# Optimization experiments

Measured on AMD Instinct MI355X. Metric: run time of the kernel, lower is better.

## Reference

```python
import jax, jax.numpy as jnp
import numpy as np

L, HID, NH, DH, OUT = 20, 512, 8, 64, 1000
NPAT, PS = 14, 16
IN_DIM = 3 * PS * PS          # 768
SEQ = NPAT * NPAT + 1         # 197
BATCH = 64
EPS = 1e-5


def _pos_embeddings(seq_len, d):
    # sin(i/10000^(j/d)) for even j, cos(i/10000^((j-1)/d)) for odd j
    i = jnp.arange(seq_len, dtype=jnp.float32)[:, None]
    j = jnp.arange(d)
    je = (j - (j % 2)).astype(jnp.float32)
    ang = i / jnp.power(10000.0, je / d)
    return jnp.where(j % 2 == 0, jnp.sin(ang), jnp.cos(ang))


def _layernorm(x, g, b):
    m = jnp.mean(x, axis=-1, keepdims=True)
    v = jnp.mean(jnp.square(x - m), axis=-1, keepdims=True)
    return (x - m) * jax.lax.rsqrt(v + EPS) * g + b


def setup_inputs() -> dict:
    key = jax.random.key(0)
    ks = jax.random.split(key, 12)
    r = lambda k, sh: jax.random.normal(k, sh, dtype=jnp.float32) * 0.02
    return {
        "x": jax.random.normal(ks[0], (BATCH, 3, 224, 224), dtype=jnp.float32),
        "embed_W": r(ks[1], (IN_DIM, HID)),
        "embed_b": jnp.zeros((HID,), jnp.float32),
        "cls": r(ks[2], (HID,)),
        "ln1_g": jnp.ones((L, HID), jnp.float32),
        "ln1_b": jnp.zeros((L, HID), jnp.float32),
        "qW": r(ks[3], (L, NH, DH, DH)),
        "qb": jnp.zeros((L, NH, DH), jnp.float32),
        "kW": r(ks[4], (L, NH, DH, DH)),
        "kb": jnp.zeros((L, NH, DH), jnp.float32),
        "vW": r(ks[5], (L, NH, DH, DH)),
        "vb": jnp.zeros((L, NH, DH), jnp.float32),
        "ln2_g": jnp.ones((L, HID), jnp.float32),
        "ln2_b": jnp.zeros((L, HID), jnp.float32),
        "mlp1_W": r(ks[6], (L, HID, 4 * HID)),
        "mlp1_b": jnp.zeros((L, 4 * HID), jnp.float32),
        "mlp2_W": r(ks[7], (L, 4 * HID, HID)),
        "mlp2_b": jnp.zeros((L, HID), jnp.float32),
        "head_W": r(ks[8], (HID, OUT)),
        "head_b": jnp.zeros((OUT,), jnp.float32),
    }


def reference(x, embed_W, embed_b, cls, ln1_g, ln1_b, qW, qb, kW, kb, vW, vb,
              ln2_g, ln2_b, mlp1_W, mlp1_b, mlp2_W, mlp2_b, head_W, head_b):
    n = x.shape[0]
    # patchify: [n,3,224,224] -> [n,196,768], flatten order (c, ph, pw)
    p = x.reshape(n, 3, NPAT, PS, NPAT, PS)
    p = p.transpose(0, 2, 4, 1, 3, 5).reshape(n, NPAT * NPAT, IN_DIM)
    tokens = p @ embed_W + embed_b                      # [n,196,HID]
    cls_tok = jnp.broadcast_to(cls, (n, 1, HID))
    h = jnp.concatenate([cls_tok, tokens], axis=1)      # [n,197,HID]
    h = h + _pos_embeddings(SEQ, HID)

    scale = 1.0 / jnp.sqrt(jnp.float32(DH))

    def step(h, params):
        (g1, b1, qw, qb_, kw, kb_, vw, vb_, g2, b2, w1, b1m, w2, b2m) = params
        y = _layernorm(h, g1, b1)                       # [n,S,HID]
        yh = y.reshape(n, SEQ, NH, DH)
        # torch Linear: out = seq @ W.T + b; qw stored as [NH, out, in]
        q = jnp.einsum('nshd,hed->nshe', yh, qw) + qb_
        k = jnp.einsum('nshd,hed->nshe', yh, kw) + kb_
        v = jnp.einsum('nshd,hed->nshe', yh, vw) + vb_
        att = jax.nn.softmax(jnp.einsum('nqhd,nkhd->nhqk', q, k) * scale, axis=-1)
        o = jnp.einsum('nhqk,nkhd->nqhd', att, v).reshape(n, SEQ, HID)
        h = h + o
        z = _layernorm(h, g2, b2)
        z = jax.nn.gelu(z @ w1 + b1m, approximate=False) @ w2 + b2m
        return h + z, None

    params = (ln1_g, ln1_b, qW, qb, kW, kb, vW, vb,
              ln2_g, ln2_b, mlp1_W, mlp1_b, mlp2_W, mlp2_b)
    h, _ = jax.lax.scan(step, h, params)
    logits = h[:, 0] @ head_W + head_b
    return jax.nn.softmax(logits, axis=-1)
```

## Files before the change

### kernel.cpp

```cpp
#include <hip/hip_runtime.h>
#include <hip/hip_bf16.h>
#include <math.h>

#define LAY 20
#define HID 512
#define NH 8
#define DH 64
#define OUTC 1000
#define SEQ 197
#define SPAD 224
#define BATCH 64
#define TT (BATCH*SEQ)
#define M2 12800
#define NPTOK (BATCH*196)
#define IN_DIM 768

typedef __attribute__((ext_vector_type(8))) short bf16x8;
typedef __attribute__((ext_vector_type(4))) float f32x4;

__device__ __forceinline__ ushort f2bf(float f){
  __hip_bfloat16 h = __float2bfloat16(f);
  return *(ushort*)&h;
}
__device__ __forceinline__ float bf2f(ushort u){
  __hip_bfloat16 h = *(__hip_bfloat16*)&u;
  return __bfloat162float(h);
}

__device__ __forceinline__ float posemb(int i, int j){
  float je = (float)(j & ~1);
  float ang = (float)i * powf(10000.0f, -je * (1.0f/(float)HID));
  return (j & 1) ? cosf(ang) : sinf(ang);
}

__device__ __forceinline__ float gelu_exact(float x){
  return 0.5f * x * (1.0f + erff(x * 0.70710678118654752f));
}

__device__ __forceinline__ void gld_lds16(const ushort* g, ushort* l){
  __builtin_amdgcn_global_load_lds((const __attribute__((address_space(1))) void*)g,
                                   (__attribute__((address_space(3))) void*)l, 16, 0, 0);
}

__global__ __launch_bounds__(512)
void pos_kernel(float* __restrict__ pos){
  int i = blockIdx.x, j = threadIdx.x;
  pos[(size_t)i*HID + j] = posemb(i, j);
}

__global__ __launch_bounds__(256)
void convt_kernel(const float* __restrict__ src, ushort* __restrict__ dst,
                  int R, int C){
  __shared__ float tile[32][33];
  const float* s = src + (size_t)blockIdx.z * R * C;
  ushort* d      = dst + (size_t)blockIdx.z * R * C;
  int r0 = blockIdx.y * 32, c0 = blockIdx.x * 32;
  int tc = threadIdx.x & 31, tr = threadIdx.x >> 5;
  #pragma unroll
  for (int i = 0; i < 4; ++i)
    tile[tr + i*8][tc] = s[(size_t)(r0 + tr + i*8)*C + c0 + tc];
  __syncthreads();
  #pragma unroll
  for (int i = 0; i < 4; ++i)
    d[(size_t)(c0 + tr + i*8)*R + r0 + tc] = f2bf(tile[tc][tr + i*8]);
}

__global__ __launch_bounds__(256)
void cvt_kernel(const float* __restrict__ src, ushort* __restrict__ dst, int count){
  int idx = blockIdx.x * 256 + threadIdx.x;
  if (idx < count) dst[idx] = f2bf(src[idx]);
}

__global__ __launch_bounds__(256)
void patchify_kernel(const float* __restrict__ x, ushort* __restrict__ p){
  int idx = blockIdx.x * 256 + threadIdx.x;
  int r   = idx / 768, cdx = idx - r * 768;
  int n   = r / 196,  pp  = r - n * 196;
  int pr  = pp / 14,  pc  = pp - pr * 14;
  int c   = cdx >> 8, rem = cdx & 255;
  int ph  = rem >> 4, pw  = rem & 15;
  p[idx] = f2bf(x[ (((size_t)(n*3 + c)*224) + pr*16 + ph)*224 + pc*16 + pw ]);
}

__global__ __launch_bounds__(512)
void cls_kernel(const float* __restrict__ cls, const float* __restrict__ pos,
                float* __restrict__ h){
  int n = blockIdx.x, e = threadIdx.x;
  h[(size_t)n*SEQ*HID + e] = cls[e] + pos[e];
}

template<int EPI>
__global__ __launch_bounds__(256, 4)
void gemm_pipe(const ushort* __restrict__ A, const ushort* __restrict__ Bt,
               const float* __restrict__ bias, void* __restrict__ Cv,
               int K, int N, int Mreal, int NBX, const float* __restrict__ pos){
  constexpr int BM = 128, BN = 128;
  constexpr int MF = 4, NF = 4;
  constexpr int TBS = 16384;
  constexpr int ES = 76;
  __shared__ char lds[2*TBS];

  int t = threadIdx.x, lane = t & 63, wave = t >> 6;
  int wr = wave >> 1, wn = wave & 1;
  int l16 = lane & 15, g = lane >> 4;

  int NB = gridDim.x;
  int q8 = NB >> 3, r8 = NB & 7;
  int xcd = blockIdx.x & 7, i8 = blockIdx.x >> 3;
  int swz = (xcd < r8 ? xcd*(q8+1) : r8*(q8+1) + (xcd-r8)*q8) + i8;
  int rb = (swz / NBX) * BM, cb = (swz % NBX) * BN;

  const int srow = t >> 2;
  const int kel  = ((t & 3) ^ ((srow >> 1) & 3)) * 8;
  const ushort* pA[2]; const ushort* pB[2];
  #pragma unroll
  for (int q = 0; q < 2; ++q){
    pA[q] = A  + (size_t)(rb + q*64 + srow)*K + kel;
    pB[q] = Bt + (size_t)(cb + q*64 + srow)*K + kel;
  }
  const int sdst = t*16;

  const int sx = (l16 >> 1) & 3;
  int aoff[MF], boff[NF];
  #pragma unroll
  for (int mf = 0; mf < MF; ++mf)
    aoff[mf] = (wr*64 + mf*16 + l16)*64 + ((g ^ sx) << 4);
  #pragma unroll
  for (int nf = 0; nf < NF; ++nf)
    boff[nf] = 8192 + (wn*64 + nf*16 + l16)*64 + ((g ^ sx) << 4);

  f32x4 acc[MF][NF];
  #pragma unroll
  for (int mf = 0; mf < MF; ++mf)
    #pragma unroll
    for (int nf = 0; nf < NF; ++nf)
      acc[mf][nf] = (f32x4){0.f,0.f,0.f,0.f};

  #pragma unroll
  for (int q = 0; q < 2; ++q){
    gld_lds16(pA[q], (ushort*)(lds + q*4096 + sdst));
    gld_lds16(pB[q], (ushort*)(lds + 8192 + q*4096 + sdst));
  }

  int NT = K / 32;
  for (int tt = 0; tt < NT; ++tt){
    const char* cur = lds + (tt & 1)*TBS;
    char* nxt = lds + ((tt & 1) ^ 1)*TBS;
    bool pf = (tt + 1 < NT);
    if (pf){
      const size_t kb = (size_t)(tt + 1) * 32;
      #pragma unroll
      for (int q = 0; q < 2; ++q){
        gld_lds16(pA[q] + kb, (ushort*)(nxt + q*4096 + sdst));
        gld_lds16(pB[q] + kb, (ushort*)(nxt + 8192 + q*4096 + sdst));
      }
      asm volatile("s_waitcnt vmcnt(4)" ::: "memory");
    } else {
      asm volatile("s_waitcnt vmcnt(0)" ::: "memory");
    }
    __builtin_amdgcn_s_barrier();

    bf16x8 af[MF], bfr[NF];
    #pragma unroll
    for (int nf = 0; nf < NF; ++nf)
      bfr[nf] = *(const bf16x8*)(cur + boff[nf]);
    #pragma unroll
    for (int mf = 0; mf < MF; ++mf)
      af[mf] = *(const bf16x8*)(cur + aoff[mf]);

    __builtin_amdgcn_s_setprio(1);
    #pragma unroll
    for (int mf = 0; mf < MF; ++mf)
      #pragma unroll
      for (int nf = 0; nf < NF; ++nf)
        acc[mf][nf] = __builtin_amdgcn_mfma_f32_16x16x32_bf16(af[mf], bfr[nf], acc[mf][nf], 0, 0, 0);
    __builtin_amdgcn_s_setprio(0);
    __builtin_amdgcn_s_barrier();
  }

  float bvv[NF];
  #pragma unroll
  for (int nf = 0; nf < NF; ++nf)
    bvv[nf] = bias[cb + wn*64 + nf*16 + l16];
  float* eps = (float*)(lds + wave*(16*ES*4));

  #pragma unroll
  for (int mf = 0; mf < MF; ++mf){
    #pragma unroll
    for (int nf = 0; nf < NF; ++nf)
      #pragma unroll
      for (int j = 0; j < 4; ++j){
        float val = acc[mf][nf][j] + bvv[nf];
        if (EPI == 1) val = gelu_exact(val);
        eps[(g*4+j)*ES + nf*16 + l16] = val;
      }
    #pragma unroll
    for (int i = 0; i < 4; ++i){
      int id = i*64 + lane;
      int r = id >> 4, c4 = id & 15;
      float4 vv = *(float4*)&eps[r*ES + c4*4];
      int grow = rb + wr*64 + mf*16 + r;
      int gcol = cb + wn*64 + c4*4;
      if (EPI == 1){
        ushort4 u;
        u.x = f2bf(vv.x); u.y = f2bf(vv.y); u.z = f2bf(vv.z); u.w = f2bf(vv.w);
        *(ushort4*)&((ushort*)Cv)[(size_t)grow*N + gcol] = u;
      } else if (EPI == 2){
        if (grow < Mreal){
          float* cp = &((float*)Cv)[(size_t)grow*N + gcol];
          float4 o = *(float4*)cp;
          o.x += vv.x; o.y += vv.y; o.z += vv.z; o.w += vv.w;
          *(float4*)cp = o;
        }
      } else {
        if (grow < Mreal){
          int bn = grow / 196, sp = grow - bn*196;
          float4 pv = *(const float4*)&pos[(size_t)(1+sp)*HID + gcol];
          vv.x += pv.x; vv.y += pv.y; vv.z += pv.z; vv.w += pv.w;
          *(float4*)&((float*)Cv)[((size_t)bn*SEQ + 1 + sp)*HID + gcol] = vv;
        }
      }
    }
  }
}

__global__ __launch_bounds__(128)
void ln_kernel(const float* __restrict__ x, const float* __restrict__ g,
               const float* __restrict__ b, ushort* __restrict__ y){
  int tok = blockIdx.x, t = threadIdx.x;
  int wave = t >> 6;
  __shared__ float red[2];
  float4 v = *(const float4*)&x[(size_t)tok*HID + t*4];
  float s = (v.x + v.y) + (v.z + v.w);
  #pragma unroll
  for (int off = 32; off; off >>= 1) s += __shfl_xor(s, off);
  if ((t & 63) == 0) red[wave] = s;
  __syncthreads();
  float mean = (red[0] + red[1]) * (1.0f/512.0f);
  __syncthreads();
  float dx = v.x - mean, dy = v.y - mean, dz = v.z - mean, dw = v.w - mean;
  s = (dx*dx + dy*dy) + (dz*dz + dw*dw);
  #pragma unroll
  for (int off = 32; off; off >>= 1) s += __shfl_xor(s, off);
  if ((t & 63) == 0) red[wave] = s;
  __syncthreads();
  float var = (red[0] + red[1]) * (1.0f/512.0f);
  float rs  = rsqrtf(var + 1e-5f);
  float4 gv = *(const float4*)&g[t*4];
  float4 bv = *(const float4*)&b[t*4];
  ushort4 o;
  o.x = f2bf(dx*rs*gv.x + bv.x);
  o.y = f2bf(dy*rs*gv.y + bv.y);
  o.z = f2bf(dz*rs*gv.z + bv.z);
  o.w = f2bf(dw*rs*gv.w + bv.w);
  *(ushort4*)&y[(size_t)tok*HID + t*4] = o;
}

__global__ __launch_bounds__(256)
void qkv_mfma(const ushort* __restrict__ y,
              const ushort* __restrict__ wqb, const ushort* __restrict__ wkb,
              const ushort* __restrict__ wvb,
              const float* __restrict__ bq, const float* __restrict__ bk,
              const float* __restrict__ bv,
              ushort* __restrict__ q, ushort* __restrict__ k,
              ushort* __restrict__ v){
  __shared__ short As[128*64];
  __shared__ short Bs[3][64*64];
  int t = threadIdx.x;
  int lane = t & 63, wave = t >> 6;
  int l16 = lane & 15, g = lane >> 4;
  int hh = blockIdx.y;
  int rb = blockIdx.x * 128;

  const ushort* Wp[3] = { wqb + (size_t)hh*64*64, wkb + (size_t)hh*64*64, wvb + (size_t)hh*64*64 };
  const float* biasp[3] = { bq + hh*64, bk + hh*64, bv + hh*64 };
  ushort* outp[3] = { q, k, v };

  int srow = t >> 3, skoff = (t & 7) * 8;
  const ushort* Ab = y + (size_t)(rb + srow)*HID + hh*64 + skoff;
  #pragma unroll
  for (int i = 0; i < 4; ++i)
    gld_lds16(Ab + (size_t)(i*32)*HID, (ushort*)&As[t*8 + i*2048]);
  #pragma unroll
  for (int p = 0; p < 3; ++p){
    const ushort* Bb = Wp[p] + (size_t)srow*64 + skoff;
    #pragma unroll
    for (int i = 0; i < 2; ++i)
      gld_lds16(Bb + (size_t)(i*32)*64, (ushort*)&Bs[p][t*8 + i*2048]);
  }
  __syncthreads();

  bf16x8 af[2][2];
  #pragma unroll
  for (int kc = 0; kc < 2; ++kc)
    #pragma unroll
    for (int m = 0; m < 2; ++m)
      af[kc][m] = *(bf16x8*)&As[(wave*32 + m*16 + l16)*64 + kc*32 + g*8];
  __syncthreads();

  ushort* eps = (ushort*)As + wave*(16*72);
  #pragma unroll
  for (int p = 0; p < 3; ++p){
    f32x4 acc[2][4];
    #pragma unroll
    for (int m = 0; m < 2; ++m)
      #pragma unroll
      for (int n = 0; n < 4; ++n)
        acc[m][n] = (f32x4){0.f,0.f,0.f,0.f};
    #pragma unroll
    for (int kc = 0; kc < 2; ++kc){
      bf16x8 bfr[4];
      #pragma unroll
      for (int n = 0; n < 4; ++n)
        bfr[n] = *(bf16x8*)&Bs[p][(n*16 + l16)*64 + kc*32 + g*8];
      #pragma unroll
      for (int m = 0; m < 2; ++m)
        #pragma unroll
        for (int n = 0; n < 4; ++n)
          acc[m][n] = __builtin_amdgcn_mfma_f32_16x16x32_bf16(af[kc][m], bfr[n], acc[m][n], 0, 0, 0);
    }
    float bvv[4];
    #pragma unroll
    for (int nd = 0; nd < 4; ++nd) bvv[nd] = biasp[p][nd*16 + l16];
    float scale = (p == 0) ? 0.125f : 1.0f;
    ushort* out = outp[p];
    #pragma unroll
    for (int mch = 0; mch < 2; ++mch){
      #pragma unroll
      for (int nd = 0; nd < 4; ++nd)
        #pragma unroll
        for (int j = 0; j < 4; ++j)
          eps[(g*4+j)*72 + nd*16 + l16] = f2bf((acc[mch][nd][j] + bvv[nd]) * scale);
      #pragma unroll
      for (int i = 0; i < 2; ++i){
        int id = i*64 + lane;
        int r = id >> 3, c8 = id & 7;
        uint4 vv = *(uint4*)&eps[r*72 + c8*8];
        int tok = rb + wave*32 + mch*16 + r;
        if (tok < TT)
          *(uint4*)&out[(size_t)tok*HID + hh*64 + c8*8] = vv;
      }
    }
  }
}

__global__ __launch_bounds__(448, 2)
void attn_kernel(const ushort* __restrict__ q, const ushort* __restrict__ k,
                 const ushort* __restrict__ v, float* __restrict__ h){
  __shared__ ushort Ks[SPAD*64];
  __shared__ ushort Vs[64*256];
  __shared__ ushort Ps[7][32*40];
  int nh = blockIdx.x;
  int n = nh >> 3, hd = nh & 7;
  int t = threadIdx.x;
  int lane = t & 63, wave = t >> 6;
  int l16 = lane & 15, g = lane >> 4;

  const ushort* kbase = k + ((size_t)n*SEQ)*HID + hd*64;
  for (int c = t; c < 224*8; c += 448){
    int s = c >> 3, c8 = (c & 7) * 8;
    int sr = s < SEQ ? s : SEQ-1;
    uint4 val = *(const uint4*)&kbase[(size_t)sr*HID + c8];
    int byte = s*128 + c8*2;
    byte ^= (s & 7) << 4;
    *(uint4*)((char*)Ks + byte) = val;
  }
  const ushort* vbase = v + ((size_t)n*SEQ)*HID + hd*64;
  for (int c = t; c < 224*8; c += 448){
    int s = c >> 3, d8 = (c & 7) * 8;
    uint4 val = {0u,0u,0u,0u};
    if (s < SEQ) val = *(const uint4*)&vbase[(size_t)s*HID + d8];
    ushort* vsp = (ushort*)Vs;
    #pragma unroll
    for (int e = 0; e < 8; ++e){
      int d = d8 + e;
      int swzi = ((d & 7) ^ ((d >> 3) & 7)) << 4;
      int byte = d*512 + ((s*2) ^ swzi);
      vsp[byte >> 1] = ((ushort*)&val)[e];
    }
  }

  int qrow0 = wave * 32;
  bf16x8 aq[2][2];
  #pragma unroll
  for (int m = 0; m < 2; ++m){
    int row = qrow0 + m*16 + l16;
    int sr = row < SEQ ? row : SEQ-1;
    const ushort* qp = q + ((size_t)n*SEQ + sr)*HID + hd*64;
    #pragma unroll
    for (int kc = 0; kc < 2; ++kc)
      aq[m][kc] = *(const bf16x8*)&qp[kc*32 + g*8];
  }
  __syncthreads();

  {
    ushort* myP = &Ps[wave][0];
    f32x4 accO[2][4];
    float mrun[2][4], lrun[2][4];
    #pragma unroll
    for (int m = 0; m < 2; ++m){
      #pragma unroll
      for (int nd = 0; nd < 4; ++nd) accO[m][nd] = (f32x4){0.f,0.f,0.f,0.f};
      #pragma unroll
      for (int j = 0; j < 4; ++j){ mrun[m][j] = -1e30f; lrun[m][j] = 0.f; }
    }

    for (int kt = 0; kt < 7; ++kt){
      f32x4 accS[2][2];
      #pragma unroll
      for (int m = 0; m < 2; ++m)
        #pragma unroll
        for (int nn = 0; nn < 2; ++nn) accS[m][nn] = (f32x4){0.f,0.f,0.f,0.f};
      #pragma unroll
      for (int kc = 0; kc < 2; ++kc){
        bf16x8 bk[2];
        #pragma unroll
        for (int nn = 0; nn < 2; ++nn){
          int srow = kt*32 + nn*16 + l16;
          int byte = srow*128 + kc*64 + g*16;
          byte ^= (srow & 7) << 4;
          bk[nn] = *(const bf16x8*)((const char*)Ks + byte);
        }
        #pragma unroll
        for (int m = 0; m < 2; ++m)
          #pragma unroll
          for (int nn = 0; nn < 2; ++nn)
            accS[m][nn] = __builtin_amdgcn_mfma_f32_16x16x32_bf16(aq[m][kc], bk[nn], accS[m][nn], 0, 0, 0);
      }
      bool kv0 = (kt*32 + l16) < SEQ;
      bool kv1 = (kt*32 + 16 + l16) < SEQ;
      #pragma unroll
      for (int m = 0; m < 2; ++m){
        #pragma unroll
        for (int j = 0; j < 4; ++j){
          float s0 = kv0 ? accS[m][0][j] : -1e30f;
          float s1 = kv1 ? accS[m][1][j] : -1e30f;
          float mx = fmaxf(s0, s1);
          mx = fmaxf(mx, __shfl_xor(mx, 1));
          mx = fmaxf(mx, __shfl_xor(mx, 2));
          mx = fmaxf(mx, __shfl_xor(mx, 4));
          mx = fmaxf(mx, __shfl_xor(mx, 8));
          float mold = mrun[m][j];
          bool skip = (mx <= mold + 8.0f);
          float mnew = skip ? mold : mx;
          mrun[m][j] = mnew;
          float p0 = __expf(s0 - mnew);
          float p1 = __expf(s1 - mnew);
          float rs = p0 + p1;
          rs += __shfl_xor(rs, 1);
          rs += __shfl_xor(rs, 2);
          rs += __shfl_xor(rs, 4);
          rs += __shfl_xor(rs, 8);
          if (skip){
            lrun[m][j] += rs;
          } else {
            float corr = __expf(mold - mnew);
            lrun[m][j] = lrun[m][j]*corr + rs;
            #pragma unroll
            for (int nd = 0; nd < 4; ++nd) accO[m][nd][j] *= corr;
          }
          int prow = m*16 + g*4 + j;
          myP[prow*40 + l16]      = f2bf(p0);
          myP[prow*40 + 16 + l16] = f2bf(p1);
        }
      }
      bf16x8 ap[2], bv[4];
      #pragma unroll
      for (int m = 0; m < 2; ++m)
        ap[m] = *(const bf16x8*)&myP[(m*16 + l16)*40 + g*8];
      #pragma unroll
      for (int nd = 0; nd < 4; ++nd){
        int d = nd*16 + l16;
        int byte = d*512 + kt*64 + g*16;
        byte ^= ((d & 7) ^ ((d >> 3) & 7)) << 4;
        bv[nd] = *(const bf16x8*)((const char*)Vs + byte);
      }
      #pragma unroll
      for (int m = 0; m < 2; ++m)
        #pragma unroll
        for (int nd = 0; nd < 4; ++nd)
          accO[m][nd] = __builtin_amdgcn_mfma_f32_16x16x32_bf16(ap[m], bv[nd], accO[m][nd], 0, 0, 0);
    }

    #pragma unroll
    for (int m = 0; m < 2; ++m){
      #pragma unroll
      for (int j = 0; j < 4; ++j){
        int row = qrow0 + m*16 + g*4 + j;
        if (row < SEQ){
          float inv = 1.0f / lrun[m][j];
          float* hp = h + ((size_t)n*SEQ + row)*HID + hd*64;
          #pragma unroll
          for (int nd = 0; nd < 4; ++nd)
            hp[nd*16 + l16] += accO[m][nd][j] * inv;
        }
      }
    }
  }
}

__global__ __launch_bounds__(256)
void head_logits(const float* __restrict__ h, const float* __restrict__ W,
                 const float* __restrict__ b, float* __restrict__ logits){
  int c0 = blockIdx.x * 8;
  __shared__ float Ws[512*8];
  int t = threadIdx.x;
  for (int i = t; i < 512*8; i += 256){
    int kx = i >> 3, c = i & 7;
    Ws[i] = W[(size_t)kx*OUTC + c0 + c];
  }
  __syncthreads();
  int n = t >> 2, g = t & 3;
  const float* hp = h + (size_t)n*SEQ*HID + g*128;
  float acc[8] = {};
  for (int kx = 0; kx < 128; ++kx){
    float hv = hp[kx];
    const float* wsr = &Ws[(g*128 + kx)*8];
    #pragma unroll
    for (int c = 0; c < 8; ++c) acc[c] += hv * wsr[c];
  }
  #pragma unroll
  for (int c = 0; c < 8; ++c){
    acc[c] += __shfl_xor(acc[c], 1);
    acc[c] += __shfl_xor(acc[c], 2);
  }
  if (g == 0){
    #pragma unroll
    for (int c = 0; c < 8; ++c)
      logits[(size_t)n*OUTC + c0 + c] = acc[c] + b[c0 + c];
  }
}

__global__ __launch_bounds__(256)
void head_softmax(const float* __restrict__ logits, float* __restrict__ out){
  int n = blockIdx.x, t = threadIdx.x;
  __shared__ float red[4];
  float v[4];
  #pragma unroll
  for (int j = 0; j < 4; ++j){
    int e = t + j*256;
    v[j] = (e < OUTC) ? logits[(size_t)n*OUTC + e] : -1e30f;
  }
  float mx = fmaxf(fmaxf(v[0], v[1]), fmaxf(v[2], v[3]));
  #pragma unroll
  for (int off = 32; off; off >>= 1) mx = fmaxf(mx, __shfl_xor(mx, off));
  if ((t & 63) == 0) red[t >> 6] = mx;
  __syncthreads();
  mx = fmaxf(fmaxf(red[0], red[1]), fmaxf(red[2], red[3]));
  __syncthreads();
  float sum = 0.f;
  #pragma unroll
  for (int j = 0; j < 4; ++j){ v[j] = __expf(v[j] - mx); sum += v[j]; }
  #pragma unroll
  for (int off = 32; off; off >>= 1) sum += __shfl_xor(sum, off);
  if ((t & 63) == 0) red[t >> 6] = sum;
  __syncthreads();
  sum = red[0] + red[1] + red[2] + red[3];
  float inv = 1.0f / sum;
  #pragma unroll
  for (int j = 0; j < 4; ++j){
    int e = t + j*256;
    if (e < OUTC) out[(size_t)n*OUTC + e] = v[j] * inv;
  }
}

extern "C" void kernel_launch(void* const* d_in, const int* in_sizes, int n_in,
                              void* d_out, int out_size, void* d_ws, size_t ws_size,
                              hipStream_t stream){
  const float* x       = (const float*)d_in[0];
  const float* embed_W = (const float*)d_in[1];
  const float* embed_b = (const float*)d_in[2];
  const float* cls     = (const float*)d_in[3];
  const float* ln1_g   = (const float*)d_in[4];
  const float* ln1_b   = (const float*)d_in[5];
  const float* qW      = (const float*)d_in[6];
  const float* qb      = (const float*)d_in[7];
  const float* kW      = (const float*)d_in[8];
  const float* kb      = (const float*)d_in[9];
  const float* vW      = (const float*)d_in[10];
  const float* vb      = (const float*)d_in[11];
  const float* ln2_g   = (const float*)d_in[12];
  const float* ln2_b   = (const float*)d_in[13];
  const float* mlp1_W  = (const float*)d_in[14];
  const float* mlp1_b  = (const float*)d_in[15];
  const float* mlp2_W  = (const float*)d_in[16];
  const float* mlp2_b  = (const float*)d_in[17];
  const float* head_W  = (const float*)d_in[18];
  const float* head_b  = (const float*)d_in[19];
  float* out = (float*)d_out;

  char* wsb = (char*)d_ws;
  float*  h   = (float*)wsb;
  ushort* y   = (ushort*)(wsb + (size_t)M2*HID*4);
  float*  logits = (float*)y;
  char*   un  = wsb + (size_t)M2*HID*4 + (size_t)M2*HID*2;
  ushort* qb_  = (ushort*)un;
  ushort* kb_  = qb_ + (size_t)TT*HID;
  ushort* vb_  = kb_ + (size_t)TT*HID;
  ushort* z1  = (ushort*)un;
  ushort* p   = (ushort*)un;
  char*   wts = un + (size_t)3*TT*HID*4;
  ushort* w1t = (ushort*)wts;
  ushort* w2t = w1t + (size_t)LAY*2048*512;
  ushort* wet = w2t + (size_t)LAY*2048*512;
  ushort* wqb = wet + (size_t)IN_DIM*HID;
  ushort* wkb = wqb + (size_t)LAY*NH*DH*DH;
  ushort* wvb = wkb + (size_t)LAY*NH*DH*DH;
  float*  pos = (float*)(wvb + (size_t)LAY*NH*DH*DH);

  pos_kernel<<<SEQ, 512, 0, stream>>>(pos);
  convt_kernel<<<dim3(2048/32, 512/32, LAY), 256, 0, stream>>>(mlp1_W, w1t, 512, 2048);
  convt_kernel<<<dim3(512/32, 2048/32, LAY), 256, 0, stream>>>(mlp2_W, w2t, 2048, 512);
  convt_kernel<<<dim3(512/32, 768/32, 1),    256, 0, stream>>>(embed_W, wet, 768, 512);
  {
    int cnt = LAY*NH*DH*DH;
    int grd = (cnt + 255)/256;
    cvt_kernel<<<grd, 256, 0, stream>>>(qW, wqb, cnt);
    cvt_kernel<<<grd, 256, 0, stream>>>(kW, wkb, cnt);
    cvt_kernel<<<grd, 256, 0, stream>>>(vW, wvb, cnt);
  }

  patchify_kernel<<<(NPTOK*IN_DIM)/256, 256, 0, stream>>>(x, p);
  cls_kernel<<<BATCH, 512, 0, stream>>>(cls, pos, h);
  gemm_pipe<3><<<(512/128)*(M2/128), 256, 0, stream>>>(
      p, wet, embed_b, h, IN_DIM, HID, NPTOK, 512/128, pos);

  for (int l = 0; l < LAY; ++l){
    ln_kernel<<<TT, 128, 0, stream>>>(h, ln1_g + l*HID, ln1_b + l*HID, y);
    qkv_mfma<<<dim3(M2/128, 8), 256, 0, stream>>>(
        y,
        wqb + (size_t)l*NH*DH*DH, wkb + (size_t)l*NH*DH*DH, wvb + (size_t)l*NH*DH*DH,
        qb + (size_t)l*HID, kb + (size_t)l*HID, vb + (size_t)l*HID,
        qb_, kb_, vb_);
    attn_kernel<<<BATCH*NH, 448, 0, stream>>>(qb_, kb_, vb_, h);
    ln_kernel<<<TT, 128, 0, stream>>>(h, ln2_g + l*HID, ln2_b + l*HID, y);
    gemm_pipe<1><<<(2048/128)*(M2/128), 256, 0, stream>>>(
        y, w1t + (size_t)l*2048*512, mlp1_b + (size_t)l*4*HID, z1,
        HID, 4*HID, TT, 2048/128, pos);
    gemm_pipe<2><<<(512/128)*(M2/128), 256, 0, stream>>>(
        z1, w2t + (size_t)l*2048*512, mlp2_b + (size_t)l*HID, h,
        4*HID, HID, TT, 512/128, pos);
  }

  head_logits<<<125, 256, 0, stream>>>(h, head_W, head_b, logits);
  head_softmax<<<BATCH, 256, 0, stream>>>(logits, out);
}
```

Baseline: 3.174 ms.

## Use 64-row tile GEMM kernel for MLP down-projection to increase block count

Adds a specialized 64x128-tile, 128-thread GEMM kernel with double-buffered LDS and residual-add epilogue, and uses it for the MLP second projection (N=512). With 128-row tiles that GEMM launched only 400 blocks; halving the M tile doubles the grid to 800 blocks for better CU occupancy on a 256-CU device. The cost is less B-tile reuse per block and more total global loads of the weight matrix.

```diff
diff --git a/kernel.cpp b/kernel.cpp
--- a/kernel.cpp
+++ b/kernel.cpp
@@ -219,6 +219,125 @@
           vv.x += pv.x; vv.y += pv.y; vv.z += pv.z; vv.w += pv.w;
           *(float4*)&((float*)Cv)[((size_t)bn*SEQ + 1 + sp)*HID + gcol] = vv;
         }
+      }
+    }
+  }
+}
+
+__global__ __launch_bounds__(128, 3)
+void gemm_pipe64(const ushort* __restrict__ A, const ushort* __restrict__ Bt,
+                 const float* __restrict__ bias, float* __restrict__ C,
+                 int K, int N, int Mreal, int NBX){
+  constexpr int MF = 2, NF = 8;
+  constexpr int TBS = 12288;
+  constexpr int ES = 140;
+  __shared__ char lds[2*TBS];
+
+  int t = threadIdx.x, lane = t & 63, wave = t >> 6;
+  int l16 = lane & 15, g = lane >> 4;
+
+  int NB = gridDim.x;
+  int q8 = NB >> 3, r8 = NB & 7;
+  int xcd = blockIdx.x & 7, i8 = blockIdx.x >> 3;
+  int swz = (xcd < r8 ? xcd*(q8+1) : r8*(q8+1) + (xcd-r8)*q8) + i8;
+  int rb = (swz / NBX) * 64, cb = (swz % NBX) * 128;
+
+  const int srow = t >> 2;
+  const int kel  = ((t & 3) ^ ((srow >> 1) & 3)) * 8;
+  const ushort* pA[2]; const ushort* pB[4];
+  #pragma unroll
+  for (int q = 0; q < 2; ++q)
+    pA[q] = A + (size_t)(rb + q*32 + srow)*K + kel;
+  #pragma unroll
+  for (int q = 0; q < 4; ++q)
+    pB[q] = Bt + (size_t)(cb + q*32 + srow)*K + kel;
+  const int sdst = t*16;
+
+  const int sx = (l16 >> 1) & 3;
+  int aoff[MF], boff[NF];
+  #pragma unroll
+  for (int mf = 0; mf < MF; ++mf)
+    aoff[mf] = (wave*32 + mf*16 + l16)*64 + ((g ^ sx) << 4);
+  #pragma unroll
+  for (int nf = 0; nf < NF; ++nf)
+    boff[nf] = 4096 + (nf*16 + l16)*64 + ((g ^ sx) << 4);
+
+  f32x4 acc[MF][NF];
+  #pragma unroll
+  for (int mf = 0; mf < MF; ++mf)
+    #pragma unroll
+    for (int nf = 0; nf < NF; ++nf)
+      acc[mf][nf] = (f32x4){0.f,0.f,0.f,0.f};
+
+  #pragma unroll
+  for (int q = 0; q < 2; ++q)
+    gld_lds16(pA[q], (ushort*)(lds + q*2048 + sdst));
+  #pragma unroll
+  for (int q = 0; q < 4; ++q)
+    gld_lds16(pB[q], (ushort*)(lds + 4096 + q*2048 + sdst));
+
+  int NT = K / 32;
+  for (int tt = 0; tt < NT; ++tt){
+    const char* cur = lds + (tt & 1)*TBS;
+    char* nxt = lds + ((tt & 1) ^ 1)*TBS;
+    bool pf = (tt + 1 < NT);
+    if (pf){
+      const size_t kb = (size_t)(tt + 1) * 32;
+      #pragma unroll
+      for (int q = 0; q < 2; ++q)
+        gld_lds16(pA[q] + kb, (ushort*)(nxt + q*2048 + sdst));
+      #pragma unroll
+      for (int q = 0; q < 4; ++q)
+        gld_lds16(pB[q] + kb, (ushort*)(nxt + 4096 + q*2048 + sdst));
+      asm volatile("s_waitcnt vmcnt(6)" ::: "memory");
+    } else {
+      asm volatile("s_waitcnt vmcnt(0)" ::: "memory");
+    }
+    __builtin_amdgcn_s_barrier();
+
+    bf16x8 af[MF], bfr[NF];
+    #pragma unroll
+    for (int nf = 0; nf < NF; ++nf)
+      bfr[nf] = *(const bf16x8*)(cur + boff[nf]);
+    #pragma unroll
+    for (int mf = 0; mf < MF; ++mf)
+      af[mf] = *(const bf16x8*)(cur + aoff[mf]);
+
+    __builtin_amdgcn_s_setprio(1);
+    #pragma unroll
+    for (int mf = 0; mf < MF; ++mf)
+      #pragma unroll
+      for (int nf = 0; nf < NF; ++nf)
+        acc[mf][nf] = __builtin_amdgcn_mfma_f32_16x16x32_bf16(af[mf], bfr[nf], acc[mf][nf], 0, 0, 0);
+    __builtin_amdgcn_s_setprio(0);
+    __builtin_amdgcn_s_barrier();
+  }
+
+  float bvv[NF];
+  #pragma unroll
+  for (int nf = 0; nf < NF; ++nf)
+    bvv[nf] = bias[cb + nf*16 + l16];
+  float* eps = (float*)(lds + wave*(16*ES*4));
+
+  #pragma unroll
+  for (int mf = 0; mf < MF; ++mf){
+    #pragma unroll
+    for (int nf = 0; nf < NF; ++nf)
+      #pragma unroll
+      for (int j = 0; j < 4; ++j)
+        eps[(g*4+j)*ES + nf*16 + l16] = acc[mf][nf][j] + bvv[nf];
+    #pragma unroll
+    for (int i = 0; i < 8; ++i){
+      int id = i*64 + lane;
+      int r = id >> 5, c4 = id & 31;
+      float4 vv = *(float4*)&eps[r*ES + c4*4];
+      int grow = rb + wave*32 + mf*16 + r;
+      int gcol = cb + c4*4;
+      if (grow < Mreal){
+        float* cp = &C[(size_t)grow*N + gcol];
+        float4 o = *(float4*)cp;
+        o.x += vv.x; o.y += vv.y; o.z += vv.z; o.w += vv.w;
+        *(float4*)cp = o;
       }
     }
   }
@@ -637,9 +756,9 @@
     gemm_pipe<1><<<(2048/128)*(M2/128), 256, 0, stream>>>(
         y, w1t + (size_t)l*2048*512, mlp1_b + (size_t)l*4*HID, z1,
         HID, 4*HID, TT, 2048/128, pos);
-    gemm_pipe<2><<<(512/128)*(M2/128), 256, 0, stream>>>(
+    gemm_pipe64<<<(512/128)*(M2/64), 128, 0, stream>>>(
         z1, w2t + (size_t)l*2048*512, mlp2_b + (size_t)l*HID, h,
-        4*HID, HID, TT, 512/128, pos);
+        4*HID, HID, TT, 512/128);
   }
 
   head_logits<<<125, 256, 0, stream>>>(h, head_W, head_b, logits);
```

New measurement: 3.521 ms. +10.9%, slower.
